# Kernel optimization log

Measured on AMD Instinct MI355X. Metric: run time of the kernel, lower is better.

The kernel has to match this reference:

```python
import jax, jax.numpy as jnp
import numpy as np
import math

B, S, D = 4, 2048, 1024
H, DK, DV = 16, 64, 64

def setup_inputs() -> dict:
    key = jax.random.key(0)
    ks = jax.random.split(key, 8)
    query = jax.random.normal(ks[0], (B, S, D), dtype=jnp.float32)
    key_t = jax.random.normal(ks[1], (B, S, D), dtype=jnp.float32)
    value = jax.random.normal(ks[2], (B, S, D), dtype=jnp.float32)
    # causal mask: True = masked (filled with -inf), broadcast over [B,H,S,S]
    mask = jnp.triu(jnp.ones((S, S), dtype=bool), k=1)[None, None, :, :]
    s = 0.02
    w_q = jax.random.normal(ks[3], (D, H * DK), dtype=jnp.float32) * s
    w_k = jax.random.normal(ks[4], (D, H * DK), dtype=jnp.float32) * s
    w_v = jax.random.normal(ks[5], (D, H * DV), dtype=jnp.float32) * s
    w_o = jax.random.normal(ks[6], (H * DV, D), dtype=jnp.float32) * s
    return {"query": query, "key": key_t, "value": value, "mask": mask,
            "w_q": w_q, "w_k": w_k, "w_v": w_v, "w_o": w_o}

def reference(query, key, value, mask, w_q, w_k, w_v, w_o):
    b, s, _ = query.shape
    # projections -> [B, H, S, dk/dv]
    q = (query @ w_q).reshape(b, s, H, DK).transpose(0, 2, 1, 3)
    k = (key @ w_k).reshape(b, s, H, DK).transpose(0, 2, 1, 3)
    v = (value @ w_v).reshape(b, s, H, DV).transpose(0, 2, 1, 3)
    scores = jnp.einsum('bhqd,bhkd->bhqk', q, k) / math.sqrt(DK)
    scores = jnp.where(mask, -jnp.inf, scores)
    attn = jax.nn.softmax(scores, axis=-1)
    out = jnp.einsum('bhqk,bhkd->bhqd', attn, v)
    out = out.transpose(0, 2, 1, 3).reshape(b, s, H * DV)
    return out @ w_o
```

## Files before the change

### kernel.cpp

```cpp
#include <hip/hip_runtime.h>
#include <hip/hip_bf16.h>

#define S_LEN 2048
#define NH 16
#define DHEAD 64
#define DMODEL 1024
#define BATCH 4

typedef __attribute__((ext_vector_type(4))) float f32x4;
typedef __attribute__((ext_vector_type(8))) short bf16x8;
typedef __attribute__((ext_vector_type(4))) short s16x4;
typedef __attribute__((ext_vector_type(4))) float fl4;
typedef __attribute__((ext_vector_type(4))) unsigned u32x4;
typedef __attribute__((ext_vector_type(2))) unsigned u32x2;

static __device__ __forceinline__ short f2bf(float f) {
  unsigned u = __builtin_bit_cast(unsigned, f);
  u += 0x7fffu + ((u >> 16) & 1u);
  return (short)(u >> 16);
}
static __device__ __forceinline__ f32x4 mfma16(bf16x8 a, bf16x8 b, f32x4 c) {
  return __builtin_amdgcn_mfma_f32_16x16x32_bf16(a, b, c, 0, 0, 0);
}
static __device__ __forceinline__ void gl_lds16(const short* g, short* l) {
  __builtin_amdgcn_global_load_lds(
      (const __attribute__((address_space(1))) unsigned*)g,
      (__attribute__((address_space(3))) unsigned*)l, 16, 0, 0);
}
static __device__ __forceinline__ unsigned cvt_pk_bf16(float lo, float hi) {
  unsigned r;
  asm("v_cvt_pk_bf16_f32 %0, %1, %2" : "=v"(r) : "v"(lo), "v"(hi));
  return r;
}

__global__ __launch_bounds__(256) void transpose_w3(
    const float* __restrict__ w0, const float* __restrict__ w1,
    const float* __restrict__ w2, short* __restrict__ o0,
    short* __restrict__ o1, short* __restrict__ o2) {
  const float* W = blockIdx.z == 0 ? w0 : blockIdx.z == 1 ? w1 : w2;
  short* O = blockIdx.z == 0 ? o0 : blockIdx.z == 1 ? o1 : o2;
  __shared__ __align__(16) short T[64][72];
  const int tid = threadIdx.x;
  const int k0 = blockIdx.y * 64, n0 = blockIdx.x * 64;
#pragma unroll
  for (int i = 0; i < 4; ++i) {
    int c = tid + i * 256;
    int kk = c >> 4, nn = (c & 15) << 2;
    fl4 v = *(const fl4*)(W + (size_t)(k0 + kk) * DMODEL + n0 + nn);
    T[nn + 0][kk] = f2bf(v.x);
    T[nn + 1][kk] = f2bf(v.y);
    T[nn + 2][kk] = f2bf(v.z);
    T[nn + 3][kk] = f2bf(v.w);
  }
  __syncthreads();
#pragma unroll
  for (int i = 0; i < 4; ++i) {
    int c = tid + i * 256;
    int nn = c >> 4, kk = (c & 15) << 2;
    *(s16x4*)(O + (size_t)(n0 + nn) * DMODEL + k0 + kk) = *(const s16x4*)&T[nn][kk];
  }
}

__global__ __launch_bounds__(256) void transpose_w1(
    const float* __restrict__ W, short* __restrict__ O) {
  __shared__ __align__(16) short T[64][72];
  const int tid = threadIdx.x;
  const int k0 = blockIdx.y * 64, n0 = blockIdx.x * 64;
#pragma unroll
  for (int i = 0; i < 4; ++i) {
    int c = tid + i * 256;
    int kk = c >> 4, nn = (c & 15) << 2;
    fl4 v = *(const fl4*)(W + (size_t)(k0 + kk) * DMODEL + n0 + nn);
    T[nn + 0][kk] = f2bf(v.x);
    T[nn + 1][kk] = f2bf(v.y);
    T[nn + 2][kk] = f2bf(v.z);
    T[nn + 3][kk] = f2bf(v.w);
  }
  __syncthreads();
#pragma unroll
  for (int i = 0; i < 4; ++i) {
    int c = tid + i * 256;
    int nn = c >> 4, kk = (c & 15) << 2;
    *(s16x4*)(O + (size_t)(n0 + nn) * DMODEL + k0 + kk) = *(const s16x4*)&T[nn][kk];
  }
}

__global__ __launch_bounds__(256) void gemm_qkv(
    const float* __restrict__ q, const float* __restrict__ k,
    const float* __restrict__ v, const short* __restrict__ Wtq,
    const short* __restrict__ Wtk, const short* __restrict__ Wtv,
    short* __restrict__ Qp, short* __restrict__ Kp, short* __restrict__ Vt,
    float qscale) {
  __shared__ __align__(16) short As[2][128 * 64];
  __shared__ __align__(16) short Bs[2][128 * 64];
  const int id = blockIdx.x;
  const int z = id >> 9;
  const int l = id & 511;
  const int cx = l & 7, j = l >> 3;
  const int n0 = (j & 7) * 128;
  const int m0 = (cx * 8 + (j >> 3)) * 128;

  const float* Af = z == 0 ? q : z == 1 ? k : v;
  const short* Bt = z == 0 ? Wtq : z == 1 ? Wtk : Wtv;
  short* Out = z == 0 ? Qp : z == 1 ? Kp : Vt;
  const float scale = z == 0 ? qscale : 1.0f;

  const int tid = threadIdx.x, lane = tid & 63, wid = tid >> 6;
  const int wm = (wid >> 1) * 64, wn = (wid & 1) * 64;
  const int lr = lane & 15, g = lane >> 4;

  f32x4 acc[4][4] = {};

  const int baseRow = tid >> 3;
  const int colOff = (((tid & 7) ^ (baseRow & 7)) << 3);
  const int slot0 = g ^ (lr & 7);

  fl4 avA[8];
  bf16x8 bvB[4];

#define LOADS(kk0) do {                                                      \
    _Pragma("unroll")                                                        \
    for (int i = 0; i < 8; ++i) {                                            \
      const int c = tid + i * 256;                                           \
      avA[i] = *(const fl4*)(Af + (size_t)(m0 + (c >> 4)) * DMODEL + (kk0) + \
                             ((c & 15) << 2));                               \
    }                                                                        \
    _Pragma("unroll")                                                        \
    for (int i = 0; i < 4; ++i)                                              \
      bvB[i] = *(const bf16x8*)(Bt + (size_t)(n0 + baseRow + i * 32) * DMODEL\
                                + (kk0) + colOff);                           \
  } while (0)

#define WRITES(bufi) do {                                                    \
    _Pragma("unroll")                                                        \
    for (int i = 0; i < 8; ++i) {                                            \
      const int c = tid + i * 256;                                           \
      const int row = c >> 4, colc = c & 15;                                 \
      u32x2 pk;                                                              \
      pk.x = cvt_pk_bf16(avA[i].x, avA[i].y);                                \
      pk.y = cvt_pk_bf16(avA[i].z, avA[i].w);                                \
      *(u32x2*)&As[bufi][row * 64 + (((colc >> 1) ^ (row & 7)) << 3) +       \
                         ((colc & 1) << 2)] = pk;                            \
    }                                                                        \
    _Pragma("unroll")                                                        \
    for (int i = 0; i < 4; ++i)                                              \
      *(bf16x8*)&Bs[bufi][(tid + i * 256) * 8] = bvB[i];                     \
  } while (0)

  LOADS(0);
  asm volatile("s_waitcnt vmcnt(0)" ::: "memory");
  WRITES(0);
  LOADS(64);
  asm volatile("s_waitcnt lgkmcnt(0)" ::: "memory");
  __builtin_amdgcn_s_barrier();

  for (int it = 0; it < 16; ++it) {
    const int cb = it & 1;
#pragma unroll
    for (int ks = 0; ks < 2; ++ks) {
      const int so = (slot0 ^ (ks << 2)) << 3;
      bf16x8 af[4], bfr[4];
#pragma unroll
      for (int t = 0; t < 4; ++t) {
        af[t] = *(const bf16x8*)&As[cb][(wm + t * 16 + lr) * 64 + so];
        bfr[t] = *(const bf16x8*)&Bs[cb][(wn + t * 16 + lr) * 64 + so];
      }
#pragma unroll
      for (int mi = 0; mi < 4; ++mi)
#pragma unroll
        for (int ni = 0; ni < 4; ++ni)
          acc[mi][ni] = mfma16(af[mi], bfr[ni], acc[mi][ni]);
    }
    if (it < 15) {
      asm volatile("s_waitcnt vmcnt(0)" ::: "memory");
      WRITES(cb ^ 1);
      if (it < 14) {
        const int knext = (it + 2) * 64;
        LOADS(knext);
      }
      asm volatile("s_waitcnt lgkmcnt(0)" ::: "memory");
      __builtin_amdgcn_s_barrier();
    }
  }
#undef LOADS
#undef WRITES

  if (z < 2) {
#pragma unroll
    for (int mi = 0; mi < 4; ++mi)
#pragma unroll
      for (int ni = 0; ni < 4; ++ni) {
        const int n = n0 + wn + ni * 16 + lr;
        const int h = n >> 6, d = n & 63;
#pragma unroll
        for (int r = 0; r < 4; ++r) {
          const int m = m0 + wm + mi * 16 + g * 4 + r;
          const int b = m >> 11, s = m & (S_LEN - 1);
          Out[(((size_t)b * NH + h) * S_LEN + s) * DHEAD + d] =
              f2bf(acc[mi][ni][r] * scale);
        }
      }
  } else {
#pragma unroll
    for (int mi = 0; mi < 4; ++mi) {
      const int mb = m0 + wm + mi * 16 + g * 4;
      const int b = mb >> 11, s = mb & (S_LEN - 1);
#pragma unroll
      for (int ni = 0; ni < 4; ++ni) {
        const int n = n0 + wn + ni * 16 + lr;
        const int h = n >> 6, d = n & 63;
        s16x4 pv;
        pv.x = f2bf(acc[mi][ni][0]);
        pv.y = f2bf(acc[mi][ni][1]);
        pv.z = f2bf(acc[mi][ni][2]);
        pv.w = f2bf(acc[mi][ni][3]);
        *(s16x4*)(Out + (((size_t)b * NH + h) * DHEAD + d) * S_LEN + s) = pv;
      }
    }
  }
}

__global__ __launch_bounds__(256) void gemm_out(
    const short* __restrict__ Ab, const short* __restrict__ Bt,
    float* __restrict__ Out) {
  __shared__ __align__(16) short As[128 * 64];
  __shared__ __align__(16) short Bs[128 * 64];
  const int id = blockIdx.x;
  const int cx = id & 7, j = id >> 3;
  const int n0 = (j & 7) * 128;
  const int m0 = (cx * 8 + (j >> 3)) * 128;

  const int tid = threadIdx.x, lane = tid & 63, wid = tid >> 6;
  const int wm = (wid >> 1) * 64, wn = (wid & 1) * 64;
  const int lr = lane & 15, g = lane >> 4;

  f32x4 acc[4][4] = {};

  const int baseRow = tid >> 3;
  const int colOff = (((tid & 7) ^ (baseRow & 7)) << 3);
  const int slot0 = g ^ (lr & 7);

  for (int k0 = 0; k0 < DMODEL; k0 += 64) {
    __syncthreads();
#pragma unroll
    for (int i = 0; i < 4; ++i) {
      const short* ga = Ab + (size_t)(m0 + baseRow + i * 32) * DMODEL + k0 + colOff;
      gl_lds16(ga, As + (tid + i * 256) * 8);
      const short* gb = Bt + (size_t)(n0 + baseRow + i * 32) * DMODEL + k0 + colOff;
      gl_lds16(gb, Bs + (tid + i * 256) * 8);
    }
    __syncthreads();

#pragma unroll
    for (int ks = 0; ks < 2; ++ks) {
      const int so = (slot0 ^ (ks << 2)) << 3;
      bf16x8 af[4], bfr[4];
#pragma unroll
      for (int t = 0; t < 4; ++t) {
        af[t] = *(const bf16x8*)&As[(wm + t * 16 + lr) * 64 + so];
        bfr[t] = *(const bf16x8*)&Bs[(wn + t * 16 + lr) * 64 + so];
      }
#pragma unroll
      for (int mi = 0; mi < 4; ++mi)
#pragma unroll
        for (int ni = 0; ni < 4; ++ni)
          acc[mi][ni] = mfma16(af[mi], bfr[ni], acc[mi][ni]);
    }
  }

#pragma unroll
  for (int mi = 0; mi < 4; ++mi)
#pragma unroll
    for (int ni = 0; ni < 4; ++ni) {
      const int n = n0 + wn + ni * 16 + lr;
#pragma unroll
      for (int r = 0; r < 4; ++r) {
        const int m = m0 + wm + mi * 16 + g * 4 + r;
        Out[(size_t)m * DMODEL + n] = acc[mi][ni][r];
      }
    }
}

static __device__ __forceinline__ void softmax_pf_static(
    f32x4 (&st)[4], bf16x8& pf0, bf16x8& pf1) {
#pragma unroll
  for (int nj = 0; nj < 4; ++nj)
#pragma unroll
    for (int r = 0; r < 4; ++r)
      st[nj][r] = exp2f(st[nj][r]);
  unsigned pw[2][4];
#pragma unroll
  for (int kc = 0; kc < 2; ++kc)
#pragma unroll
    for (int jj = 0; jj < 2; ++jj) {
      unsigned a = cvt_pk_bf16(st[2 * kc][2 * jj], st[2 * kc][2 * jj + 1]);
      unsigned bb = cvt_pk_bf16(st[2 * kc + 1][2 * jj], st[2 * kc + 1][2 * jj + 1]);
      asm("v_permlane32_swap_b32 %0, %1" : "+v"(a), "+v"(bb));
      asm("v_permlane16_swap_b32 %0, %1" : "+v"(a), "+v"(bb));
      pw[kc][jj] = a;
      pw[kc][jj + 2] = bb;
    }
  u32x4 w0 = {pw[0][0], pw[0][1], pw[0][2], pw[0][3]};
  u32x4 w1 = {pw[1][0], pw[1][1], pw[1][2], pw[1][3]};
  pf0 = __builtin_bit_cast(bf16x8, w0);
  pf1 = __builtin_bit_cast(bf16x8, w1);
}

static __device__ __forceinline__ void attn_epilogue(
    f32x4 (&ot)[4], float lsum, int b, int h, int qa, int g,
    short* __restrict__ AO) {
  const float inv = 1.f / lsum;
  short* dst = AO + ((size_t)b * S_LEN + qa) * DMODEL + h * DHEAD + (g << 2);
#pragma unroll
  for (int nd = 0; nd < 4; ++nd) {
    s16x4 pv;
    pv.x = f2bf(ot[nd][0] * inv);
    pv.y = f2bf(ot[nd][1] * inv);
    pv.z = f2bf(ot[nd][2] * inv);
    pv.w = f2bf(ot[nd][3] * inv);
    *(s16x4*)(dst + nd * 16) = pv;
  }
}

__global__ __launch_bounds__(256) void attn9(
    const short* __restrict__ Qp, const short* __restrict__ Kp,
    const short* __restrict__ VT, short* __restrict__ AO) {
  __shared__ __align__(16) short KV[2][8192];
  const int tid = threadIdx.x, lane = tid & 63, wid = tid >> 6;
  const int lr = lane & 15, g = lane >> 4;
  const int id = blockIdx.x;
  const int xcd = id & 7;
  const int bh = xcd * 8 + ((id >> 3) & 7);
  const int sg = 31 - (id >> 6);
  const int t = sg * 4 + wid;
  const short* Qb = Qp + (size_t)bh * S_LEN * DHEAD;
  const short* Kb = Kp + (size_t)bh * S_LEN * DHEAD;
  const short* Vb = VT + (size_t)bh * DHEAD * S_LEN;
  const int b = bh >> 4, h = bh & 15;

  const int NT = sg + 1;
  const int q0 = t << 4;
  const int qa = q0 + lr;

  const int row1 = tid >> 3;
  const int col1 = (tid & 7) ^ (row1 & 7);
  const int kOff1 = row1 * DHEAD + col1 * 8;
  const int vOff1 = row1 * S_LEN + col1 * 8;

#define STAGE9(bufi, kvv) do {                                      \
    const short* ks_ = Kb + (size_t)(kvv) * DHEAD + kOff1;          \
    gl_lds16(ks_,               &KV[bufi][0] + tid * 8);            \
    gl_lds16(ks_ + 32 * DHEAD,  &KV[bufi][2048] + tid * 8);         \
    const short* vs_ = Vb + (kvv) + vOff1;                          \
    gl_lds16(vs_,               &KV[bufi][4096] + tid * 8);         \
    gl_lds16(vs_ + 32 * S_LEN,  &KV[bufi][6144] + tid * 8);         \
  } while (0)

  const int slot0 = g ^ (lr & 7);
  const int fOff0 = lr * 64 + slot0 * 8;
  const int fOff1 = lr * 64 + (slot0 ^ 4) * 8;

  bf16x8 qf[2];
  qf[0] = *(const bf16x8*)(Qb + (size_t)qa * DHEAD + (g << 3));
  qf[1] = *(const bf16x8*)(Qb + (size_t)qa * DHEAD + 32 + (g << 3));

  bf16x8 ones;
#pragma unroll
  for (int i = 0; i < 8; ++i) ones[i] = (short)0x3F80;

  f32x4 ot[4] = {};
  f32x4 lacc = {};

  STAGE9(0, 0);

  for (int it = 0; it < NT; ++it) {
    const int kv0 = it << 6;
    const int cb = it & 1;
    if (it + 1 < NT) {
      STAGE9(cb ^ 1, kv0 + 64);
      asm volatile("s_waitcnt vmcnt(4)" ::: "memory");
    } else {
      asm volatile("s_waitcnt vmcnt(0)" ::: "memory");
    }
    __builtin_amdgcn_s_barrier();

    const short* kb = &KV[cb][0];
    const short* vb = &KV[cb][4096];

    f32x4 st[4] = {};
    __builtin_amdgcn_s_setprio(1);
#pragma unroll
    for (int nj = 0; nj < 4; ++nj) {
      bf16x8 k0 = *(const bf16x8*)(kb + fOff0 + nj * 1024);
      bf16x8 k1 = *(const bf16x8*)(kb + fOff1 + nj * 1024);
      st[nj] = mfma16(k0, qf[0], st[nj]);
      st[nj] = mfma16(k1, qf[1], st[nj]);
    }
    __builtin_amdgcn_s_setprio(0);
    if (it == NT - 1) {
#pragma unroll
      for (int nj = 0; nj < 4; ++nj)
#pragma unroll
        for (int r = 0; r < 4; ++r)
          if (kv0 + nj * 16 + (g << 2) + r > qa) st[nj][r] = -1e30f;
    }
    bf16x8 pf0, pf1;
    softmax_pf_static(st, pf0, pf1);
    __builtin_amdgcn_s_setprio(1);
    lacc = mfma16(ones, pf0, lacc);
    lacc = mfma16(ones, pf1, lacc);
#pragma unroll
    for (int nd = 0; nd < 4; ++nd) {
      bf16x8 v0 = *(const bf16x8*)(vb + fOff0 + nd * 1024);
      bf16x8 v1 = *(const bf16x8*)(vb + fOff1 + nd * 1024);
      ot[nd] = mfma16(v0, pf0, ot[nd]);
      ot[nd] = mfma16(v1, pf1, ot[nd]);
    }
    __builtin_amdgcn_s_setprio(0);
    __builtin_amdgcn_s_barrier();
  }
#undef STAGE9

  attn_epilogue(ot, lacc[0], b, h, qa, g, AO);
}

extern "C" void kernel_launch(void* const* d_in, const int* in_sizes, int n_in,
                              void* d_out, int out_size, void* d_ws, size_t ws_size,
                              hipStream_t stream) {
  const float* query = (const float*)d_in[0];
  const float* key   = (const float*)d_in[1];
  const float* value = (const float*)d_in[2];
  const float* w_q = (const float*)d_in[4];
  const float* w_k = (const float*)d_in[5];
  const float* w_v = (const float*)d_in[6];
  const float* w_o = (const float*)d_in[7];

  const size_t QKV = (size_t)BATCH * NH * S_LEN * DHEAD;
  short* Qp = (short*)d_ws;
  short* Kp = Qp + QKV;
  short* Vt = Kp + QKV;
  short* AO = Vt + QKV;
  short* Wto = Qp;
  short* Wtq = (short*)d_out;
  short* Wtk = Wtq + (size_t)DMODEL * DMODEL;
  short* Wtv = Wtk + (size_t)DMODEL * DMODEL;

  dim3 blk(256);
  const float qscale = 0.125f * 1.4426950408889634f;

  transpose_w3<<<dim3(16, 16, 3), blk, 0, stream>>>(w_q, w_k, w_v, Wtq, Wtk, Wtv);
  gemm_qkv<<<dim3(1536), blk, 0, stream>>>(
      query, key, value, Wtq, Wtk, Wtv, Qp, Kp, Vt, qscale);
  attn9<<<dim3(2048), blk, 0, stream>>>(Qp, Kp, Vt, AO);
  transpose_w1<<<dim3(16, 16), blk, 0, stream>>>(w_o, Wto);
  gemm_out<<<dim3(512), blk, 0, stream>>>(AO, Wto, (float*)d_out);
}
```

Before: 172.9 us.

## Load V fragments directly from global into registers, stage only K in LDS

The attention kernel no longer stages V tiles through shared memory. Each wave now loads its V fragments straight from global memory into registers, issuing the loads after the QK^T MFMAs so that softmax can hide their latency. The K double-buffer prefetch is moved after those loads, and the trailing per-iteration barrier is removed, leaving one barrier per iteration. This halves LDS usage and cuts barrier traffic, which may raise occupancy. In exchange the four waves of a block load the same V tile redundantly through the cache, and global-load latency is more exposed inside the loop.

```diff
diff --git a/kernel.cpp b/kernel.cpp
--- a/kernel.cpp
+++ b/kernel.cpp
@@ -322,10 +322,10 @@
   }
 }
 
-__global__ __launch_bounds__(256) void attn9(
+__global__ __launch_bounds__(256) void attn11(
     const short* __restrict__ Qp, const short* __restrict__ Kp,
     const short* __restrict__ VT, short* __restrict__ AO) {
-  __shared__ __align__(16) short KV[2][8192];
+  __shared__ __align__(16) short Kl[2][4096];
   const int tid = threadIdx.x, lane = tid & 63, wid = tid >> 6;
   const int lr = lane & 15, g = lane >> 4;
   const int id = blockIdx.x;
@@ -345,15 +345,11 @@
   const int row1 = tid >> 3;
   const int col1 = (tid & 7) ^ (row1 & 7);
   const int kOff1 = row1 * DHEAD + col1 * 8;
-  const int vOff1 = row1 * S_LEN + col1 * 8;
-
-#define STAGE9(bufi, kvv) do {                                      \
+
+#define STAGEK(bufi, kvv) do {                                      \
     const short* ks_ = Kb + (size_t)(kvv) * DHEAD + kOff1;          \
-    gl_lds16(ks_,               &KV[bufi][0] + tid * 8);            \
-    gl_lds16(ks_ + 32 * DHEAD,  &KV[bufi][2048] + tid * 8);         \
-    const short* vs_ = Vb + (kvv) + vOff1;                          \
-    gl_lds16(vs_,               &KV[bufi][4096] + tid * 8);         \
-    gl_lds16(vs_ + 32 * S_LEN,  &KV[bufi][6144] + tid * 8);         \
+    gl_lds16(ks_,               &Kl[bufi][0] + tid * 8);            \
+    gl_lds16(ks_ + 32 * DHEAD,  &Kl[bufi][2048] + tid * 8);         \
   } while (0)
 
   const int slot0 = g ^ (lr & 7);
@@ -371,21 +367,15 @@
   f32x4 ot[4] = {};
   f32x4 lacc = {};
 
-  STAGE9(0, 0);
+  STAGEK(0, 0);
 
   for (int it = 0; it < NT; ++it) {
     const int kv0 = it << 6;
     const int cb = it & 1;
-    if (it + 1 < NT) {
-      STAGE9(cb ^ 1, kv0 + 64);
-      asm volatile("s_waitcnt vmcnt(4)" ::: "memory");
-    } else {
-      asm volatile("s_waitcnt vmcnt(0)" ::: "memory");
-    }
+    asm volatile("s_waitcnt vmcnt(0)" ::: "memory");
     __builtin_amdgcn_s_barrier();
 
-    const short* kb = &KV[cb][0];
-    const short* vb = &KV[cb][4096];
+    const short* kb = &Kl[cb][0];
 
     f32x4 st[4] = {};
     __builtin_amdgcn_s_setprio(1);
@@ -397,6 +387,15 @@
       st[nj] = mfma16(k1, qf[1], st[nj]);
     }
     __builtin_amdgcn_s_setprio(0);
+    bf16x8 vf[4][2];
+    const short* vp0 = Vb + (size_t)lr * S_LEN + kv0 + (g << 3);
+#pragma unroll
+    for (int nd = 0; nd < 4; ++nd) {
+      vf[nd][0] = *(const bf16x8*)(vp0 + (size_t)nd * 16 * S_LEN);
+      vf[nd][1] = *(const bf16x8*)(vp0 + (size_t)nd * 16 * S_LEN + 32);
+    }
+    asm volatile("" ::: "memory");
+    if (it + 1 < NT) STAGEK(cb ^ 1, kv0 + 64);
     if (it == NT - 1) {
 #pragma unroll
       for (int nj = 0; nj < 4; ++nj)
@@ -411,15 +410,12 @@
     lacc = mfma16(ones, pf1, lacc);
 #pragma unroll
     for (int nd = 0; nd < 4; ++nd) {
-      bf16x8 v0 = *(const bf16x8*)(vb + fOff0 + nd * 1024);
-      bf16x8 v1 = *(const bf16x8*)(vb + fOff1 + nd * 1024);
-      ot[nd] = mfma16(v0, pf0, ot[nd]);
-      ot[nd] = mfma16(v1, pf1, ot[nd]);
+      ot[nd] = mfma16(vf[nd][0], pf0, ot[nd]);
+      ot[nd] = mfma16(vf[nd][1], pf1, ot[nd]);
     }
     __builtin_amdgcn_s_setprio(0);
-    __builtin_amdgcn_s_barrier();
-  }
-#undef STAGE9
+  }
+#undef STAGEK
 
   attn_epilogue(ot, lacc[0], b, h, qa, g, AO);
 }
@@ -451,7 +447,7 @@
   transpose_w3<<<dim3(16, 16, 3), blk, 0, stream>>>(w_q, w_k, w_v, Wtq, Wtk, Wtv);
   gemm_qkv<<<dim3(1536), blk, 0, stream>>>(
       query, key, value, Wtq, Wtk, Wtv, Qp, Kp, Vt, qscale);
-  attn9<<<dim3(2048), blk, 0, stream>>>(Qp, Kp, Vt, AO);
+  attn11<<<dim3(2048), blk, 0, stream>>>(Qp, Kp, Vt, AO);
   transpose_w1<<<dim3(16, 16), blk, 0, stream>>>(w_o, Wto);
   gemm_out<<<dim3(512), blk, 0, stream>>>(AO, Wto, (float*)d_out);
 }
```

Result: slower. 238.6 us (+38.0%).

## Shrink attention KV tile to 32 keys with per-wave causal skipping

Applied to the files above, without the earlier changes.

The attention kernel now streams K/V in 32-key blocks instead of 64 and lets each wave skip compute for blocks past its own causal limit, while the block still loads every tile needed by its last wave. This cuts the wasted QK/PV MFMA work on masked diagonal tiles and halves LDS use per buffer. The cost is twice as many loop iterations, barriers and global-to-LDS stages, with less MFMA work per barrier to hide latency. The V layout in LDS is remapped so that a 64-dim by 32-key tile fits the new swizzled layout.

```diff
diff --git a/kernel.cpp b/kernel.cpp
--- a/kernel.cpp
+++ b/kernel.cpp
@@ -281,31 +281,6 @@
     }
 }
 
-static __device__ __forceinline__ void softmax_pf_static(
-    f32x4 (&st)[4], bf16x8& pf0, bf16x8& pf1) {
-#pragma unroll
-  for (int nj = 0; nj < 4; ++nj)
-#pragma unroll
-    for (int r = 0; r < 4; ++r)
-      st[nj][r] = exp2f(st[nj][r]);
-  unsigned pw[2][4];
-#pragma unroll
-  for (int kc = 0; kc < 2; ++kc)
-#pragma unroll
-    for (int jj = 0; jj < 2; ++jj) {
-      unsigned a = cvt_pk_bf16(st[2 * kc][2 * jj], st[2 * kc][2 * jj + 1]);
-      unsigned bb = cvt_pk_bf16(st[2 * kc + 1][2 * jj], st[2 * kc + 1][2 * jj + 1]);
-      asm("v_permlane32_swap_b32 %0, %1" : "+v"(a), "+v"(bb));
-      asm("v_permlane16_swap_b32 %0, %1" : "+v"(a), "+v"(bb));
-      pw[kc][jj] = a;
-      pw[kc][jj + 2] = bb;
-    }
-  u32x4 w0 = {pw[0][0], pw[0][1], pw[0][2], pw[0][3]};
-  u32x4 w1 = {pw[1][0], pw[1][1], pw[1][2], pw[1][3]};
-  pf0 = __builtin_bit_cast(bf16x8, w0);
-  pf1 = __builtin_bit_cast(bf16x8, w1);
-}
-
 static __device__ __forceinline__ void attn_epilogue(
     f32x4 (&ot)[4], float lsum, int b, int h, int qa, int g,
     short* __restrict__ AO) {
@@ -322,10 +297,10 @@
   }
 }
 
-__global__ __launch_bounds__(256) void attn9(
+__global__ __launch_bounds__(256) void attn12(
     const short* __restrict__ Qp, const short* __restrict__ Kp,
     const short* __restrict__ VT, short* __restrict__ AO) {
-  __shared__ __align__(16) short KV[2][8192];
+  __shared__ __align__(16) short KV[2][4096];
   const int tid = threadIdx.x, lane = tid & 63, wid = tid >> 6;
   const int lr = lane & 15, g = lane >> 4;
   const int id = blockIdx.x;
@@ -338,27 +313,31 @@
   const short* Vb = VT + (size_t)bh * DHEAD * S_LEN;
   const int b = bh >> 4, h = bh & 15;
 
-  const int NT = sg + 1;
+  const int NTw = (t + 2) >> 1;
+  const int NTblk = 2 * sg + 2;
   const int q0 = t << 4;
   const int qa = q0 + lr;
 
   const int row1 = tid >> 3;
-  const int col1 = (tid & 7) ^ (row1 & 7);
-  const int kOff1 = row1 * DHEAD + col1 * 8;
-  const int vOff1 = row1 * S_LEN + col1 * 8;
-
-#define STAGE9(bufi, kvv) do {                                      \
-    const short* ks_ = Kb + (size_t)(kvv) * DHEAD + kOff1;          \
-    gl_lds16(ks_,               &KV[bufi][0] + tid * 8);            \
-    gl_lds16(ks_ + 32 * DHEAD,  &KV[bufi][2048] + tid * 8);         \
-    const short* vs_ = Vb + (kvv) + vOff1;                          \
-    gl_lds16(vs_,               &KV[bufi][4096] + tid * 8);         \
-    gl_lds16(vs_ + 32 * S_LEN,  &KV[bufi][6144] + tid * 8);         \
+  const int sl1 = (tid & 7) ^ (row1 & 7);
+  const int kOff1 = row1 * DHEAD + sl1 * 8;
+  const int vOff1 = (row1 + 32 * (sl1 >> 2)) * S_LEN + (sl1 & 3) * 8;
+
+#define STAGE12(bufi, kvv) do {                                     \
+    gl_lds16(Kb + (size_t)(kvv) * DHEAD + kOff1,                    \
+             &KV[bufi][0] + tid * 8);                               \
+    gl_lds16(Vb + vOff1 + (kvv),                                    \
+             &KV[bufi][2048] + tid * 8);                            \
   } while (0)
 
   const int slot0 = g ^ (lr & 7);
-  const int fOff0 = lr * 64 + slot0 * 8;
-  const int fOff1 = lr * 64 + (slot0 ^ 4) * 8;
+  const int kf0 = lr * 64 + slot0 * 8;
+  const int kf1 = lr * 64 + (slot0 ^ 4) * 8;
+  int vOffR[4];
+#pragma unroll
+  for (int nd = 0; nd < 4; ++nd)
+    vOffR[nd] = (16 * (nd & 1) + lr) * 64 +
+                ((((nd >> 1) << 2) | g) ^ (lr & 7)) * 8;
 
   bf16x8 qf[2];
   qf[0] = *(const bf16x8*)(Qb + (size_t)qa * DHEAD + (g << 3));
@@ -371,55 +350,69 @@
   f32x4 ot[4] = {};
   f32x4 lacc = {};
 
-  STAGE9(0, 0);
-
-  for (int it = 0; it < NT; ++it) {
-    const int kv0 = it << 6;
+  STAGE12(0, 0);
+
+  for (int it = 0; it < NTblk; ++it) {
+    const int kv0 = it << 5;
     const int cb = it & 1;
-    if (it + 1 < NT) {
-      STAGE9(cb ^ 1, kv0 + 64);
-      asm volatile("s_waitcnt vmcnt(4)" ::: "memory");
+    if (it + 1 < NTblk) {
+      STAGE12(cb ^ 1, kv0 + 32);
+      asm volatile("s_waitcnt vmcnt(2)" ::: "memory");
     } else {
       asm volatile("s_waitcnt vmcnt(0)" ::: "memory");
     }
     __builtin_amdgcn_s_barrier();
 
-    const short* kb = &KV[cb][0];
-    const short* vb = &KV[cb][4096];
-
-    f32x4 st[4] = {};
-    __builtin_amdgcn_s_setprio(1);
-#pragma unroll
-    for (int nj = 0; nj < 4; ++nj) {
-      bf16x8 k0 = *(const bf16x8*)(kb + fOff0 + nj * 1024);
-      bf16x8 k1 = *(const bf16x8*)(kb + fOff1 + nj * 1024);
-      st[nj] = mfma16(k0, qf[0], st[nj]);
-      st[nj] = mfma16(k1, qf[1], st[nj]);
-    }
-    __builtin_amdgcn_s_setprio(0);
-    if (it == NT - 1) {
-#pragma unroll
-      for (int nj = 0; nj < 4; ++nj)
+    if (it < NTw) {
+      const short* kb = &KV[cb][0];
+      const short* vb = &KV[cb][2048];
+
+      f32x4 st[2] = {};
+      __builtin_amdgcn_s_setprio(1);
+#pragma unroll
+      for (int nj = 0; nj < 2; ++nj) {
+        bf16x8 k0 = *(const bf16x8*)(kb + kf0 + nj * 1024);
+        bf16x8 k1 = *(const bf16x8*)(kb + kf1 + nj * 1024);
+        st[nj] = mfma16(k0, qf[0], st[nj]);
+        st[nj] = mfma16(k1, qf[1], st[nj]);
+      }
+      __builtin_amdgcn_s_setprio(0);
+      if (it == NTw - 1) {
+#pragma unroll
+        for (int nj = 0; nj < 2; ++nj)
+#pragma unroll
+          for (int r = 0; r < 4; ++r)
+            if (kv0 + nj * 16 + (g << 2) + r > qa) st[nj][r] = -1e30f;
+      }
+#pragma unroll
+      for (int nj = 0; nj < 2; ++nj)
 #pragma unroll
         for (int r = 0; r < 4; ++r)
-          if (kv0 + nj * 16 + (g << 2) + r > qa) st[nj][r] = -1e30f;
-    }
-    bf16x8 pf0, pf1;
-    softmax_pf_static(st, pf0, pf1);
-    __builtin_amdgcn_s_setprio(1);
-    lacc = mfma16(ones, pf0, lacc);
-    lacc = mfma16(ones, pf1, lacc);
-#pragma unroll
-    for (int nd = 0; nd < 4; ++nd) {
-      bf16x8 v0 = *(const bf16x8*)(vb + fOff0 + nd * 1024);
-      bf16x8 v1 = *(const bf16x8*)(vb + fOff1 + nd * 1024);
-      ot[nd] = mfma16(v0, pf0, ot[nd]);
-      ot[nd] = mfma16(v1, pf1, ot[nd]);
-    }
-    __builtin_amdgcn_s_setprio(0);
+          st[nj][r] = exp2f(st[nj][r]);
+      unsigned pw[4];
+#pragma unroll
+      for (int jj = 0; jj < 2; ++jj) {
+        unsigned a = cvt_pk_bf16(st[0][2 * jj], st[0][2 * jj + 1]);
+        unsigned bb = cvt_pk_bf16(st[1][2 * jj], st[1][2 * jj + 1]);
+        asm("v_permlane32_swap_b32 %0, %1" : "+v"(a), "+v"(bb));
+        asm("v_permlane16_swap_b32 %0, %1" : "+v"(a), "+v"(bb));
+        pw[jj] = a;
+        pw[jj + 2] = bb;
+      }
+      u32x4 w0 = {pw[0], pw[1], pw[2], pw[3]};
+      bf16x8 pf0 = __builtin_bit_cast(bf16x8, w0);
+      __builtin_amdgcn_s_setprio(1);
+      lacc = mfma16(ones, pf0, lacc);
+#pragma unroll
+      for (int nd = 0; nd < 4; ++nd) {
+        bf16x8 vf = *(const bf16x8*)(vb + vOffR[nd]);
+        ot[nd] = mfma16(vf, pf0, ot[nd]);
+      }
+      __builtin_amdgcn_s_setprio(0);
+    }
     __builtin_amdgcn_s_barrier();
   }
-#undef STAGE9
+#undef STAGE12
 
   attn_epilogue(ot, lacc[0], b, h, qa, g, AO);
 }
@@ -451,7 +444,7 @@
   transpose_w3<<<dim3(16, 16, 3), blk, 0, stream>>>(w_q, w_k, w_v, Wtq, Wtk, Wtv);
   gemm_qkv<<<dim3(1536), blk, 0, stream>>>(
       query, key, value, Wtq, Wtk, Wtv, Qp, Kp, Vt, qscale);
-  attn9<<<dim3(2048), blk, 0, stream>>>(Qp, Kp, Vt, AO);
+  attn12<<<dim3(2048), blk, 0, stream>>>(Qp, Kp, Vt, AO);
   transpose_w1<<<dim3(16, 16), blk, 0, stream>>>(w_o, Wto);
   gemm_out<<<dim3(512), blk, 0, stream>>>(AO, Wto, (float*)d_out);
 }
```

Result: slower. 178.2 us (+3.0%).
